# Kernel optimization log

Hardware: AMD Instinct MI355X
Metric: run time of the kernel (lower is better)

Reference implementation:

```python
import jax, jax.numpy as jnp
import numpy as np

N, E, NG, H, BD, L, B = 4000, 50000, 12, 128, 128, 2, 100

def _gelu(x):
    return jax.nn.gelu(x, approximate=False)

def forward(pos, vel, charges, grid0, rand_SO3, batch, edge_index,
            W_basis1, b_basis1, W_basis2, b_basis2,
            W_fbasis1, b_fbasis1, W_fbasis2, b_fbasis2,
            W_embed, W_conv, W_fiber, b_conv, ln_gamma, ln_beta,
            W_ff1, b_ff1, W_ff2, b_ff2, W_ro1, b_ro1, W_ro2, b_ro2):
    n_nodes = pos.shape[0]
    n_graphs = rand_SO3.shape[0]
    n = grid0.shape[0]
    src, dst = edge_index[0], edge_index[1]
    # per-graph randomly rotated S2 grid
    grid_graph = jnp.einsum('bij,nj->bni', rand_SO3, grid0)    # [B,n,3]
    grid_node = grid_graph[batch]                               # [N,n,3]
    grid_edge = grid_node[src]                                  # [E,n,3]
    # R3S2 Euclidean invariants (separable): parallel + perpendicular parts of rel_pos wrt each grid orientation
    rel = pos[src] - pos[dst]                                   # [E,3]
    inv1 = jnp.einsum('ed,end->en', rel, grid_edge)[..., None]  # [E,n,1]
    inv2 = jnp.linalg.norm(rel[:, None, :] - inv1 * grid_edge, axis=-1, keepdims=True)
    cp = (charges[src] * charges[dst])[:, None, :]              # [E,1,1]
    ei = jnp.concatenate([inv1, inv2, jnp.broadcast_to(cp, inv1.shape)], -1)  # [E,n,3]
    # PolynomialFeatures(degree=2): [x, flatten(x outer x)] -> 3+9=12
    ei_poly = jnp.concatenate([ei, (ei[..., :, None] * ei[..., None, :]).reshape(ei.shape[:-1] + (9,))], -1)
    basis = _gelu(_gelu(ei_poly @ W_basis1 + b_basis1) @ W_basis2 + b_basis2)  # [E,n,BD]
    # fiber invariants: pairwise grid dot products (rotation cancels) -> [n,n,1]; poly deg 2 -> [n,n,2]
    fi = jnp.sum(grid0[:, None, :] * grid0[None, :, :], -1, keepdims=True)
    fi_poly = jnp.concatenate([fi, fi * fi], -1)
    fiber_basis = _gelu(_gelu(fi_poly @ W_fbasis1 + b_fbasis1) @ W_fbasis2 + b_fbasis2)  # [n,n,BD]
    # node features projected to sphere
    ones = jnp.ones((n_nodes, 1), pos.dtype)
    cnt = jax.ops.segment_sum(ones, batch, num_segments=n_graphs)
    mean_pos = jax.ops.segment_sum(pos, batch, num_segments=n_graphs) / jnp.maximum(cnt, 1.0)
    rel_pos = pos - mean_pos[batch]
    v_sph = jnp.einsum('nd,nkd->nk', vel, grid_node)[..., None]
    p_sph = jnp.einsum('nd,nkd->nk', rel_pos, grid_node)[..., None]
    c_sph = jnp.broadcast_to(charges[:, None, :], (n_nodes, n, 1))
    vn = jnp.linalg.norm(vel, axis=-1, keepdims=True)
    vn_sph = jnp.broadcast_to(vn[:, None, :], (n_nodes, n, 1))
    x = jnp.concatenate([v_sph, p_sph, c_sph, vn_sph], -1) @ W_embed  # [N,n,H]
    # SeparableBundleConvNext stack
    for l in range(W_conv.shape[0]):
        kern = basis @ W_conv[l]                                       # [E,n,H]
        x1 = jax.ops.segment_sum(x[src] * kern, dst, num_segments=n_nodes)  # depthwise spatial conv + scatter-add
        fk = fiber_basis @ W_fiber[l]                                  # [n,n,H]
        x2 = jnp.einsum('boc,poc->bpc', x1, fk) / n + b_conv[l]        # depthwise fiber conv
        mu = jnp.mean(x2, -1, keepdims=True)
        var = jnp.mean((x2 - mu) ** 2, -1, keepdims=True)
        h = (x2 - mu) / jnp.sqrt(var + 1e-5) * ln_gamma[l] + ln_beta[l]
        h = _gelu(h @ W_ff1[l] + b_ff1[l]) @ W_ff2[l] + b_ff2[l]
        x = x + h
    y = _gelu(x @ W_ro1 + b_ro1) @ W_ro2 + b_ro2                       # [N,n,1]
    return jnp.mean(grid_node * y, axis=-2)                            # sphere2vec -> [N,3]

def setup_inputs():
    key = jax.random.key(0)
    ks = jax.random.split(key, 24)
    f = jnp.float32
    # deterministic uniform-ish S2 grid (fibonacci sphere)
    i = np.arange(NG) + 0.5
    phi = np.arccos(1.0 - 2.0 * i / NG)
    th = np.pi * (1.0 + 5.0 ** 0.5) * i
    grid0 = jnp.asarray(np.stack([np.sin(phi) * np.cos(th), np.sin(phi) * np.sin(th), np.cos(phi)], -1), f)
    # random SO(3) per graph via unit quaternions
    q = jax.random.normal(ks[0], (B, 4), f)
    q = q / jnp.linalg.norm(q, axis=-1, keepdims=True)
    w, xq, yq, zq = q[:, 0], q[:, 1], q[:, 2], q[:, 3]
    R = jnp.stack([
        jnp.stack([1 - 2 * (yq ** 2 + zq ** 2), 2 * (xq * yq - zq * w), 2 * (xq * zq + yq * w)], -1),
        jnp.stack([2 * (xq * yq + zq * w), 1 - 2 * (xq ** 2 + zq ** 2), 2 * (yq * zq - xq * w)], -1),
        jnp.stack([2 * (xq * zq - yq * w), 2 * (yq * zq + xq * w), 1 - 2 * (xq ** 2 + yq ** 2)], -1)], -2)
    s = 0.05
    return dict(
        pos=jax.random.normal(ks[1], (N, 3), f),
        vel=jax.random.normal(ks[2], (N, 3), f),
        charges=jax.random.normal(ks[3], (N, 1), f),
        batch=jnp.sort(jax.random.randint(ks[4], (N,), 0, B)),
        edge_index=jax.random.randint(ks[5], (2, E), 0, N),
        grid0=grid0, rand_SO3=R,
        W_basis1=jax.random.normal(ks[6], (12, H), f) * s, b_basis1=jnp.zeros((H,), f),
        W_basis2=jax.random.normal(ks[7], (H, BD), f) * s, b_basis2=jnp.zeros((BD,), f),
        W_fbasis1=jax.random.normal(ks[8], (2, H), f) * s, b_fbasis1=jnp.zeros((H,), f),
        W_fbasis2=jax.random.normal(ks[9], (H, BD), f) * s, b_fbasis2=jnp.zeros((BD,), f),
        W_embed=jax.random.normal(ks[10], (4, H), f) * s,
        W_conv=jax.random.normal(ks[11], (L, BD, H), f) * s,
        W_fiber=jax.random.normal(ks[12], (L, BD, H), f) * s,
        b_conv=jnp.zeros((L, H), f),
        ln_gamma=jnp.ones((L, H), f), ln_beta=jnp.zeros((L, H), f),
        W_ff1=jax.random.normal(ks[13], (L, H, 4 * H), f) * s, b_ff1=jnp.zeros((L, 4 * H), f),
        W_ff2=jax.random.normal(ks[14], (L, 4 * H, H), f) * s, b_ff2=jnp.zeros((L, H), f),
        W_ro1=jax.random.normal(ks[15], (H, H), f) * s, b_ro1=jnp.zeros((H,), f),
        W_ro2=jax.random.normal(ks[16], (H, 1), f) * s, b_ro2=jnp.zeros((1,), f),
    )

def reference(pos, vel, charges, batch, edge_index, grid0, rand_SO3,
              W_basis1, b_basis1, W_basis2, b_basis2,
              W_fbasis1, b_fbasis1, W_fbasis2, b_fbasis2,
              W_embed, W_conv, W_fiber, b_conv, ln_gamma, ln_beta,
              W_ff1, b_ff1, W_ff2, b_ff2, W_ro1, b_ro1, W_ro2, b_ro2):
    return forward(pos, vel, charges, grid0, rand_SO3, batch, edge_index,
                   W_basis1, b_basis1, W_basis2, b_basis2,
                   W_fbasis1, b_fbasis1, W_fbasis2, b_fbasis2,
                   W_embed, W_conv, W_fiber, b_conv, ln_gamma, ln_beta,
                   W_ff1, b_ff1, W_ff2, b_ff2, W_ro1, b_ro1, W_ro2, b_ro2)
```

## Files before the change

### kernel.cpp

```cpp
#include <hip/hip_runtime.h>

typedef unsigned short u16;
typedef short s16x8 __attribute__((ext_vector_type(8)));
typedef float f32x4 __attribute__((ext_vector_type(4)));

constexpr int NNODES = 4000;
constexpr int NEDGES = 50000;
constexpr int NGRID  = 12;
constexpr int HD     = 128;
constexpr int H4     = 512;
constexpr int NLAY   = 2;

constexpr size_t OFF_GN   = 0;
constexpr size_t OFF_PS   = 144000;
constexpr size_t OFF_CNT  = 144304;
constexpr size_t OFF_FK   = 144512;
constexpr size_t OFF_X    = 181376;
constexpr size_t OFF_X1   = 6325376;
constexpr size_t OFF_WB   = 12469376;
constexpr size_t OFF_ROWP = 12625024;
constexpr size_t OFF_DEG  = 12629032;
constexpr size_t OFF_CUR  = 12633032;
constexpr size_t OFF_ESRT = 12637032;
constexpr size_t OFF_EIPB = 12687032;
constexpr size_t OFF_W1T  = 17487416;
constexpr size_t OFF_SRCS = 17489464;
constexpr size_t OFF_END_SLOW = 17539464;
constexpr size_t OFF_BAS  = 17539464;
constexpr size_t KERN_F   = 38400000;
constexpr size_t OFF_END_FAST  = OFF_BAS + KERN_F;
constexpr size_t OFF_END_DUAL  = OFF_BAS + 2*KERN_F;

constexpr size_t WB_W2T = 0;
constexpr size_t WB_WCT = 16384;
constexpr size_t WB_F1T = 49152;
constexpr size_t WB_F2T = 180224;

__device__ __forceinline__ u16 f2bf(float f){
  union { float f; unsigned int i; } v; v.f = f;
  unsigned int x = v.i;
  x += 0x7fffu + ((x >> 16) & 1u);
  return (u16)(x >> 16);
}
__device__ __forceinline__ float bf2f(u16 u){
  union { unsigned int i; float f; } v; v.i = ((unsigned int)u) << 16; return v.f;
}
__device__ __forceinline__ float gelu_f(float x){
  float z = fabsf(x) * 0.70710678118654752f;
  float t = 1.0f / (1.0f + 0.3275911f * z);
  float p = t*(0.254829592f + t*(-0.284496736f + t*(1.421413741f + t*(-1.453152027f + t*1.061405429f))));
  float erfc_z = p * __expf(-z*z);
  float phi = (x >= 0.0f) ? (1.0f - 0.5f*erfc_z) : (0.5f*erfc_z);
  return x * phi;
}
__device__ __forceinline__ float waveReduceSum(float v){
  #pragma unroll
  for(int off = 32; off > 0; off >>= 1) v += __shfl_xor(v, off, 64);
  return v;
}
__device__ __forceinline__ f32x4 mfma16(s16x8 a, s16x8 b, f32x4 c){
  return __builtin_amdgcn_mfma_f32_16x16x32_bf16(a, b, c, 0, 0, 0);
}

__global__ void k_stats(const float* __restrict__ pos, const int* __restrict__ batch,
                        float* __restrict__ possum, float* __restrict__ pcnt){
  int n = blockIdx.x * 256 + threadIdx.x;
  if(n >= NNODES) return;
  int b = batch[n];
  atomicAdd(&possum[b*3+0], pos[n*3+0]);
  atomicAdd(&possum[b*3+1], pos[n*3+1]);
  atomicAdd(&possum[b*3+2], pos[n*3+2]);
  atomicAdd(&pcnt[b], 1.0f);
}

__global__ void k_gridnode(const float* __restrict__ g0, const float* __restrict__ R,
                           const int* __restrict__ batch, float* __restrict__ grid_node){
  int idx = blockIdx.x * 256 + threadIdx.x;
  if(idx >= NNODES*NGRID) return;
  int n = idx / NGRID, k = idx % NGRID;
  int b = batch[n];
  float g[3];
  #pragma unroll
  for(int j=0;j<3;j++) g[j] = g0[k*3+j];
  #pragma unroll
  for(int i=0;i<3;i++){
    float s = 0.f;
    #pragma unroll
    for(int j=0;j<3;j++) s += R[b*9+i*3+j] * g[j];
    grid_node[idx*3+i] = s;
  }
}

__global__ __launch_bounds__(128) void k_embed(
    const float* __restrict__ pos, const float* __restrict__ vel, const float* __restrict__ charges,
    const int* __restrict__ batch, const float* __restrict__ possum, const float* __restrict__ pcnt,
    const float* __restrict__ grid_node, const float* __restrict__ W_embed, float* __restrict__ x)
{
  int n = blockIdx.x; int t = threadIdx.x;
  __shared__ float feats[NGRID][4];
  __shared__ float sgn[NGRID][3];
  if(t < 36) sgn[t/3][t%3] = grid_node[n*36 + t];
  __syncthreads();
  if(t < NGRID){
    int b = batch[n];
    float inv = 1.0f / fmaxf(pcnt[b], 1.0f);
    float v0=vel[n*3], v1=vel[n*3+1], v2=vel[n*3+2];
    float p0=pos[n*3]   - possum[b*3]*inv;
    float p1=pos[n*3+1] - possum[b*3+1]*inv;
    float p2=pos[n*3+2] - possum[b*3+2]*inv;
    float g0=sgn[t][0], g1=sgn[t][1], g2=sgn[t][2];
    feats[t][0] = v0*g0 + v1*g1 + v2*g2;
    feats[t][1] = p0*g0 + p1*g1 + p2*g2;
    feats[t][2] = charges[n];
    feats[t][3] = sqrtf(v0*v0 + v1*v1 + v2*v2);
  }
  __syncthreads();
  float w0=W_embed[0*HD+t], w1=W_embed[1*HD+t];
  float w2=W_embed[2*HD+t], w3=W_embed[3*HD+t];
  #pragma unroll
  for(int k=0;k<NGRID;k++)
    x[(n*NGRID+k)*HD + t] = feats[k][0]*w0 + feats[k][1]*w1 + feats[k][2]*w2 + feats[k][3]*w3;
}

__global__ __launch_bounds__(128) void k_fiber(
    const float* __restrict__ g0, const float* __restrict__ Wf1, const float* __restrict__ bfb1,
    const float* __restrict__ Wf2, const float* __restrict__ bfb2, const float* __restrict__ W_fiber,
    float* __restrict__ fk)
{
  int po = blockIdx.x; int p = po / NGRID, o = po % NGRID; int c = threadIdx.x;
  __shared__ float st[HD];
  __shared__ float sfb[HD];
  float fi = 0.f;
  #pragma unroll
  for(int j=0;j<3;j++) fi += g0[p*3+j] * g0[o*3+j];
  float f2 = fi*fi;
  st[c] = gelu_f(fi*Wf1[c] + f2*Wf1[HD+c] + bfb1[c]);
  __syncthreads();
  float a = bfb2[c];
  for(int j=0;j<HD;j++) a += st[j] * Wf2[j*HD+c];
  sfb[c] = gelu_f(a);
  __syncthreads();
  for(int l=0;l<NLAY;l++){
    float s = 0.f;
    for(int j=0;j<HD;j++) s += sfb[j] * W_fiber[l*HD*HD + j*HD + c];
    fk[(l*144 + po)*HD + c] = s;
  }
}

__global__ void k_prep(const float* __restrict__ W_b2, const float* __restrict__ W_b1,
                       const float* __restrict__ W_conv, const float* __restrict__ W_ff1,
                       const float* __restrict__ W_ff2,
                       u16* __restrict__ W2T, u16* __restrict__ W1T, u16* __restrict__ WCT,
                       u16* __restrict__ F1T, u16* __restrict__ F2T){
  int idx = blockIdx.x * 256 + threadIdx.x;
  if(idx < 16384){
    int r = idx >> 7, c = idx & 127;
    W2T[c*128 + r] = f2bf(W_b2[idx]);
    return;
  }
  idx -= 16384;
  if(idx < 4096){
    int c = idx >> 5, f = idx & 31;
    W1T[idx] = (f < 12) ? f2bf(W_b1[f*HD + c]) : (u16)0;
    return;
  }
  idx -= 4096;
  if(idx < 32768){
    int l = idx >> 14, j = idx & 16383;
    int r = j >> 7, c = j & 127;
    WCT[l*16384 + c*128 + r] = f2bf(W_conv[l*16384 + j]);
    return;
  }
  idx -= 32768;
  if(idx < 131072){
    int l = idx >> 16, j = idx & 65535;
    int r = j / 512, c = j % 512;
    F1T[l*65536 + c*128 + r] = f2bf(W_ff1[l*65536 + j]);
    return;
  }
  idx -= 131072;
  if(idx < 131072){
    int l = idx >> 16, j = idx & 65535;
    int r = j / 128, c = j % 128;
    F2T[l*65536 + c*512 + r] = f2bf(W_ff2[l*65536 + j]);
  }
}

__global__ void k_prepro(const float* __restrict__ W_ro1, u16* __restrict__ RO1T){
  int idx = blockIdx.x * 256 + threadIdx.x;
  if(idx >= 16384) return;
  int r = idx >> 7, c = idx & 127;
  RO1T[c*128 + r] = f2bf(W_ro1[idx]);
}

__global__ void k_deg(const int* __restrict__ eidx, int* __restrict__ deg){
  int e = blockIdx.x * 256 + threadIdx.x;
  if(e >= NEDGES) return;
  atomicAdd(&deg[eidx[NEDGES + e]], 1);
}

__global__ __launch_bounds__(256) void k_scan(const int* __restrict__ deg, int* __restrict__ rowptr){
  int t = threadIdx.x;
  __shared__ int part[256];
  int base = t * 16;
  int lp[16]; int s = 0;
  #pragma unroll
  for(int i=0;i<16;i++){
    int idx = base + i;
    int v = (idx < NNODES) ? deg[idx] : 0;
    lp[i] = s; s += v;
  }
  part[t] = s;
  __syncthreads();
  for(int off=1; off<256; off<<=1){
    int v2 = (t >= off) ? part[t-off] : 0;
    __syncthreads();
    part[t] += v2;
    __syncthreads();
  }
  int excl = part[t] - s;
  #pragma unroll
  for(int i=0;i<16;i++){
    int idx = base + i;
    if(idx < NNODES) rowptr[idx] = excl + lp[i];
  }
  if(t == 255) rowptr[NNODES] = part[255];
}

__global__ void k_bucket(const int* __restrict__ eidx, const int* __restrict__ rowptr,
                         int* __restrict__ cur, int* __restrict__ esorted, int* __restrict__ srcs){
  int e = blockIdx.x * 256 + threadIdx.x;
  if(e >= NEDGES) return;
  int d = eidx[NEDGES + e];
  int p = atomicAdd(&cur[d], 1);
  int slot = rowptr[d] + p;
  esorted[slot] = e;
  srcs[slot] = eidx[e];
}

__global__ void k_einv(const int* __restrict__ esorted, const int* __restrict__ eidx,
                       const float* __restrict__ pos, const float* __restrict__ charges,
                       const float* __restrict__ grid_node, u16* __restrict__ eipb){
  int row = blockIdx.x * 256 + threadIdx.x;
  if(row >= NEDGES*NGRID) return;
  int p = row / NGRID, kg = row - p*NGRID;
  int e = esorted[p];
  int sr = eidx[e], ds = eidx[NEDGES + e];
  float r0 = pos[sr*3]   - pos[ds*3];
  float r1 = pos[sr*3+1] - pos[ds*3+1];
  float r2 = pos[sr*3+2] - pos[ds*3+2];
  float cp = charges[sr] * charges[ds];
  float g0 = grid_node[sr*36 + kg*3];
  float g1 = grid_node[sr*36 + kg*3 + 1];
  float g2 = grid_node[sr*36 + kg*3 + 2];
  float inv1 = r0*g0 + r1*g1 + r2*g2;
  float d0 = r0 - inv1*g0, d1 = r1 - inv1*g1, d2 = r2 - inv1*g2;
  float inv2 = sqrtf(d0*d0 + d1*d1 + d2*d2);
  float ei[3] = {inv1, inv2, cp};
  s16x8 lo, hi;
  #pragma unroll
  for(int i=0;i<3;i++) lo[i] = (short)f2bf(ei[i]);
  lo[3] = (short)f2bf(ei[0]*ei[0]);
  lo[4] = (short)f2bf(ei[0]*ei[1]);
  lo[5] = (short)f2bf(ei[0]*ei[2]);
  lo[6] = (short)f2bf(ei[1]*ei[0]);
  lo[7] = (short)f2bf(ei[1]*ei[1]);
  hi[0] = (short)f2bf(ei[1]*ei[2]);
  hi[1] = (short)f2bf(ei[2]*ei[0]);
  hi[2] = (short)f2bf(ei[2]*ei[1]);
  hi[3] = (short)f2bf(ei[2]*ei[2]);
  hi[4] = 0; hi[5] = 0; hi[6] = 0; hi[7] = 0;
  *(s16x8*)&eipb[(size_t)row*16]     = lo;
  *(s16x8*)&eipb[(size_t)row*16 + 8] = hi;
}

constexpr int T1S = 136;

__global__ __launch_bounds__(256) void k_kern(
    const u16* __restrict__ eipb, const u16* __restrict__ W1T,
    const float* __restrict__ b1, const float* __restrict__ b2,
    const u16* __restrict__ W2T, const u16* __restrict__ WCT,
    u16* __restrict__ kern, int nl, size_t kstride)
{
  int t = threadIdx.x;
  int lane = t & 63, w = t >> 6, quad = lane >> 4, l16 = lane & 15;
  size_t R0 = (size_t)blockIdx.x * 64;
  __shared__ __align__(16) u16 s_buf[64*T1S];

  float b1v[2], b2v[2];
  #pragma unroll
  for(int nt=0;nt<2;nt++){
    b1v[nt] = b1[(2*w+nt)*16 + l16];
    b2v[nt] = b2[(2*w+nt)*16 + l16];
  }
  const s16x8 zvec = {0,0,0,0,0,0,0,0};

  {
    f32x4 a1[4][2];
    #pragma unroll
    for(int mt=0;mt<4;mt++)
      #pragma unroll
      for(int nt=0;nt<2;nt++) a1[mt][nt] = (f32x4){0.f,0.f,0.f,0.f};
    s16x8 Af[4];
    #pragma unroll
    for(int mt=0;mt<4;mt++){
      s16x8 v = *(const s16x8*)&eipb[(R0 + mt*16 + l16)*16 + (quad&1)*8];
      if(quad >= 2) v = zvec;
      Af[mt] = v;
    }
    #pragma unroll
    for(int nt=0;nt<2;nt++){
      s16x8 Bf = *(const s16x8*)&W1T[((2*w+nt)*16 + l16)*32 + quad*8];
      #pragma unroll
      for(int mt=0;mt<4;mt++) a1[mt][nt] = mfma16(Af[mt], Bf, a1[mt][nt]);
    }
    #pragma unroll
    for(int mt=0;mt<4;mt++)
      #pragma unroll
      for(int nt=0;nt<2;nt++)
        #pragma unroll
        for(int i=0;i<4;i++)
          s_buf[(mt*16 + quad*4 + i)*T1S + (2*w+nt)*16 + l16] = f2bf(gelu_f(a1[mt][nt][i] + b1v[nt]));
  }
  __syncthreads();
  f32x4 a2[4][2];
  #pragma unroll
  for(int mt=0;mt<4;mt++)
    #pragma unroll
    for(int nt=0;nt<2;nt++) a2[mt][nt] = (f32x4){0.f,0.f,0.f,0.f};
  #pragma unroll
  for(int ks=0; ks<4; ks++){
    s16x8 Af[4];
    #pragma unroll
    for(int mt=0;mt<4;mt++)
      Af[mt] = *(const s16x8*)&s_buf[(mt*16 + l16)*T1S + ks*32 + quad*8];
    #pragma unroll
    for(int nt=0;nt<2;nt++){
      s16x8 Bf = *(const s16x8*)&W2T[((2*w+nt)*16 + l16)*HD + ks*32 + quad*8];
      #pragma unroll
      for(int mt=0;mt<4;mt++) a2[mt][nt] = mfma16(Af[mt], Bf, a2[mt][nt]);
    }
  }
  __syncthreads();
  #pragma unroll
  for(int mt=0;mt<4;mt++)
    #pragma unroll
    for(int nt=0;nt<2;nt++)
      #pragma unroll
      for(int i=0;i<4;i++)
        s_buf[(mt*16 + quad*4 + i)*T1S + (2*w+nt)*16 + l16] = f2bf(gelu_f(a2[mt][nt][i] + b2v[nt]));
  __syncthreads();
  for(int l=0; l<nl; l++){
    f32x4 a3[4][2];
    #pragma unroll
    for(int mt=0;mt<4;mt++)
      #pragma unroll
      for(int nt=0;nt<2;nt++) a3[mt][nt] = (f32x4){0.f,0.f,0.f,0.f};
    #pragma unroll
    for(int ks=0; ks<4; ks++){
      s16x8 Af[4];
      #pragma unroll
      for(int mt=0;mt<4;mt++)
        Af[mt] = *(const s16x8*)&s_buf[(mt*16 + l16)*T1S + ks*32 + quad*8];
      #pragma unroll
      for(int nt=0;nt<2;nt++){
        s16x8 Bf = *(const s16x8*)&WCT[l*16384 + ((2*w+nt)*16 + l16)*HD + ks*32 + quad*8];
        #pragma unroll
        for(int mt=0;mt<4;mt++) a3[mt][nt] = mfma16(Af[mt], Bf, a3[mt][nt]);
      }
    }
    #pragma unroll
    for(int mt=0;mt<4;mt++)
      #pragma unroll
      for(int nt=0;nt<2;nt++)
        #pragma unroll
        for(int i=0;i<4;i++)
          kern[l*kstride + (R0 + mt*16 + quad*4 + i)*HD + (2*w+nt)*16 + l16] = f2bf(a3[mt][nt][i]);
  }
}

__global__ __launch_bounds__(256) void k_gather(
    const u16* __restrict__ kern, const float* __restrict__ x,
    const int* __restrict__ rowptr, const int* __restrict__ srcs,
    const float* __restrict__ fkl, const float* __restrict__ bconv,
    const float* __restrict__ gamma, const float* __restrict__ beta,
    u16* __restrict__ hout)
{
  int n = blockIdx.x, t = threadIdx.x;
  int c = t & 127, half = t >> 7;
  int w = t >> 6, lane = t & 63;
  __shared__ float raw[NGRID*HD];
  __shared__ float red[4][6], red2[4][6];
  int base = rowptr[n];
  int d = rowptr[n+1] - base;
  float acc[6] = {0.f,0.f,0.f,0.f,0.f,0.f};
  int srcn = (d > 0) ? srcs[base] : 0;
  for(int e=0; e<d; e++){
    int nsrc = (e+1 < d) ? srcs[base+e+1] : 0;
    const u16*   kp = &kern[((size_t)(base+e)*NGRID + half*6)*HD + c];
    const float* xp = &x[((size_t)srcn*NGRID + half*6)*HD + c];
    #pragma unroll
    for(int kk=0;kk<6;kk++)
      acc[kk] += bf2f(kp[kk*HD]) * xp[kk*HD];
    srcn = nsrc;
  }
  #pragma unroll
  for(int kk=0;kk<6;kk++)
    raw[(half*6+kk)*HD + c] = acc[kk];
  __syncthreads();
  float bc = bconv[c];
  float v[6];
  #pragma unroll
  for(int kk=0;kk<6;kk++){
    int p = half*6 + kk;
    float a = 0.f;
    #pragma unroll
    for(int o=0;o<NGRID;o++)
      a += raw[o*HD + c] * fkl[(p*NGRID+o)*HD + c];
    v[kk] = a * (1.0f/12.0f) + bc;
  }
  #pragma unroll
  for(int kk=0;kk<6;kk++){
    float s = waveReduceSum(v[kk]);
    if(lane == 0) red[w][kk] = s;
  }
  __syncthreads();
  float dd[6];
  #pragma unroll
  for(int kk=0;kk<6;kk++){
    float mu = (red[half*2][kk] + red[half*2+1][kk]) * (1.0f/128.0f);
    dd[kk] = v[kk] - mu;
    float s2 = waveReduceSum(dd[kk]*dd[kk]);
    if(lane == 0) red2[w][kk] = s2;
  }
  __syncthreads();
  float ga = gamma[c], be = beta[c];
  #pragma unroll
  for(int kk=0;kk<6;kk++){
    float var = (red2[half*2][kk] + red2[half*2+1][kk]) * (1.0f/128.0f);
    float inv = 1.0f / sqrtf(var + 1e-5f);
    hout[((size_t)n*NGRID + half*6 + kk)*HD + c] = f2bf(dd[kk] * inv * ga + be);
  }
}

__global__ __launch_bounds__(256) void k_ff1(
    const u16* __restrict__ F1T, const float* __restrict__ bf1,
    const u16* __restrict__ hin, u16* __restrict__ h4)
{
  int t = threadIdx.x;
  size_t r0 = (size_t)blockIdx.x * 32;
  int lane = t & 63, w = t >> 6, quad = lane >> 4, l16 = lane & 15;
  __shared__ __align__(16) u16 sxh[32*T1S];
  for(int i=t; i<32*HD/8; i+=256){
    int r = (i*8) >> 7, cc = (i*8) & 127;
    *(s16x8*)&sxh[r*T1S + cc] = *(const s16x8*)&hin[r0*HD + (size_t)i*8];
  }
  __syncthreads();
  f32x4 acc[2][8];
  #pragma unroll
  for(int mt=0;mt<2;mt++)
    #pragma unroll
    for(int j=0;j<8;j++) acc[mt][j] = (f32x4){0.f,0.f,0.f,0.f};
  #pragma unroll
  for(int ks=0; ks<4; ks++){
    s16x8 Af0 = *(const s16x8*)&sxh[l16*T1S + ks*32 + quad*8];
    s16x8 Af1 = *(const s16x8*)&sxh[(16 + l16)*T1S + ks*32 + quad*8];
    #pragma unroll
    for(int j=0;j<8;j++){
      int nt = w*8 + j;
      s16x8 Bf = *(const s16x8*)&F1T[((size_t)(nt*16 + l16))*HD + ks*32 + quad*8];
      acc[0][j] = mfma16(Af0, Bf, acc[0][j]);
      acc[1][j] = mfma16(Af1, Bf, acc[1][j]);
    }
  }
  #pragma unroll
  for(int j=0;j<8;j++){
    int col = (w*8+j)*16 + l16;
    float bv = bf1[col];
    #pragma unroll
    for(int mt=0;mt<2;mt++)
      #pragma unroll
      for(int i=0;i<4;i++){
        int row = mt*16 + quad*4 + i;
        h4[(r0 + row)*H4 + col] = f2bf(gelu_f(acc[mt][j][i] + bv));
      }
  }
}

__global__ __launch_bounds__(256) void k_ff2(
    const u16* __restrict__ F2T, const float* __restrict__ bf2,
    const u16* __restrict__ h4, float* __restrict__ x)
{
  int t = threadIdx.x;
  size_t r0 = (size_t)blockIdx.x * 32;
  int lane = t & 63, w = t >> 6, quad = lane >> 4, l16 = lane & 15;
  f32x4 acc[2][2];
  #pragma unroll
  for(int mt=0;mt<2;mt++)
    #pragma unroll
    for(int j=0;j<2;j++) acc[mt][j] = (f32x4){0.f,0.f,0.f,0.f};
  for(int ks=0; ks<16; ks++){
    s16x8 Af0 = *(const s16x8*)&h4[(r0 + l16)*H4 + ks*32 + quad*8];
    s16x8 Af1 = *(const s16x8*)&h4[(r0 + 16 + l16)*H4 + ks*32 + quad*8];
    #pragma unroll
    for(int j=0;j<2;j++){
      int nt = w*2 + j;
      s16x8 Bf = *(const s16x8*)&F2T[((size_t)(nt*16 + l16))*H4 + ks*32 + quad*8];
      acc[0][j] = mfma16(Af0, Bf, acc[0][j]);
      acc[1][j] = mfma16(Af1, Bf, acc[1][j]);
    }
  }
  #pragma unroll
  for(int j=0;j<2;j++){
    int col = (w*2+j)*16 + l16;
    float bv = bf2[col];
    #pragma unroll
    for(int mt=0;mt<2;mt++)
      #pragma unroll
      for(int i=0;i<4;i++){
        size_t row = r0 + mt*16 + quad*4 + i;
        x[row*HD + col] += acc[mt][j][i] + bv;
      }
  }
}

__global__ __launch_bounds__(256) void k_conv_slow(
    const u16* __restrict__ eipb, const u16* __restrict__ W1T,
    const float* __restrict__ b1, const float* __restrict__ b2,
    const u16* __restrict__ W2T, const u16* __restrict__ WCT,
    const float* __restrict__ x,
    const int* __restrict__ rowptr, const int* __restrict__ srcs,
    float* __restrict__ x1o)
{
  int n = blockIdx.x; int t = threadIdx.x;
  int lane = t & 63, w = t >> 6, quad = lane >> 4, l16 = lane & 15;

  __shared__ __align__(16) u16 s_t1h[48*T1S];
  __shared__ __align__(16) u16 s_bas[48*T1S];
  __shared__ __align__(16) float accLDS[NGRID*HD];

  int base = rowptr[n];
  int d = rowptr[n+1] - base;

  float b1v[2], b2v[2];
  #pragma unroll
  for(int nt=0;nt<2;nt++){
    b1v[nt] = b1[(2*w+nt)*16 + l16];
    b2v[nt] = b2[(2*w+nt)*16 + l16];
  }

  for(int i=t; i<NGRID*HD; i+=256) accLDS[i] = 0.f;
  __syncthreads();

  f32x4 accv[3][2];
  #pragma unroll
  for(int mt=0;mt<3;mt++)
    #pragma unroll
    for(int nt=0;nt<2;nt++) accv[mt][nt] = (f32x4){0.f,0.f,0.f,0.f};

  const s16x8 zvec = {0,0,0,0,0,0,0,0};

  for(int ch=0; ch<d; ch+=4){
    size_t rowb = (size_t)(base + ch) * NGRID;
    s16x8 Af1[3];
    #pragma unroll
    for(int mt=0;mt<3;mt++){
      s16x8 v = *(const s16x8*)&eipb[(rowb + mt*16 + l16)*16 + (quad&1)*8];
      if(quad >= 2) v = zvec;
      Af1[mt] = v;
    }
    float xv[3][4][2];
    #pragma unroll
    for(int mt=0;mt<3;mt++)
      #pragma unroll
      for(int i=0;i<4;i++){
        int row = mt*16 + quad*4 + i;
        int e = row / 12;
        int k = row - e*12;
        int ei2 = base + ch + e;
        int srcn = srcs[min(ei2, NEDGES-1)];
        float m = (ch + e < d) ? 1.0f : 0.0f;
        const float* xp = &x[((size_t)srcn*NGRID + k)*HD + l16];
        #pragma unroll
        for(int nt=0;nt<2;nt++)
          xv[mt][i][nt] = xp[(2*w+nt)*16] * m;
      }
    {
      f32x4 a1[3][2];
      #pragma unroll
      for(int mt=0;mt<3;mt++)
        #pragma unroll
        for(int nt=0;nt<2;nt++) a1[mt][nt] = (f32x4){0.f,0.f,0.f,0.f};
      #pragma unroll
      for(int nt=0;nt<2;nt++){
        s16x8 Bf = *(const s16x8*)&W1T[((2*w+nt)*16 + l16)*32 + quad*8];
        #pragma unroll
        for(int mt=0;mt<3;mt++) a1[mt][nt] = mfma16(Af1[mt], Bf, a1[mt][nt]);
      }
      #pragma unroll
      for(int mt=0;mt<3;mt++)
        #pragma unroll
        for(int nt=0;nt<2;nt++)
          #pragma unroll
          for(int i=0;i<4;i++)
            s_t1h[(mt*16 + quad*4 + i)*T1S + (2*w+nt)*16 + l16] = f2bf(gelu_f(a1[mt][nt][i] + b1v[nt]));
    }
    __syncthreads();
    {
      f32x4 a2[3][2];
      #pragma unroll
      for(int mt=0;mt<3;mt++)
        #pragma unroll
        for(int nt=0;nt<2;nt++) a2[mt][nt] = (f32x4){0.f,0.f,0.f,0.f};
      #pragma unroll
      for(int ks=0; ks<4; ks++){
        s16x8 Af[3];
        #pragma unroll
        for(int mt=0;mt<3;mt++)
          Af[mt] = *(const s16x8*)&s_t1h[(mt*16 + l16)*T1S + ks*32 + quad*8];
        #pragma unroll
        for(int nt=0;nt<2;nt++){
          s16x8 Bf = *(const s16x8*)&W2T[((2*w+nt)*16 + l16)*HD + ks*32 + quad*8];
          #pragma unroll
          for(int mt=0;mt<3;mt++) a2[mt][nt] = mfma16(Af[mt], Bf, a2[mt][nt]);
        }
      }
      #pragma unroll
      for(int mt=0;mt<3;mt++)
        #pragma unroll
        for(int nt=0;nt<2;nt++)
          #pragma unroll
          for(int i=0;i<4;i++)
            s_bas[(mt*16 + quad*4 + i)*T1S + (2*w+nt)*16 + l16] = f2bf(gelu_f(a2[mt][nt][i] + b2v[nt]));
    }
    __syncthreads();
    {
      f32x4 a3[3][2];
      #pragma unroll
      for(int mt=0;mt<3;mt++)
        #pragma unroll
        for(int nt=0;nt<2;nt++) a3[mt][nt] = (f32x4){0.f,0.f,0.f,0.f};
      #pragma unroll
      for(int ks=0; ks<4; ks++){
        s16x8 Af[3];
        #pragma unroll
        for(int mt=0;mt<3;mt++)
          Af[mt] = *(const s16x8*)&s_bas[(mt*16 + l16)*T1S + ks*32 + quad*8];
        #pragma unroll
        for(int nt=0;nt<2;nt++){
          s16x8 Bf = *(const s16x8*)&WCT[((2*w+nt)*16 + l16)*HD + ks*32 + quad*8];
          #pragma unroll
          for(int mt=0;mt<3;mt++) a3[mt][nt] = mfma16(Af[mt], Bf, a3[mt][nt]);
        }
      }
      #pragma unroll
      for(int mt=0;mt<3;mt++)
        #pragma unroll
        for(int nt=0;nt<2;nt++)
          #pragma unroll
          for(int i=0;i<4;i++)
            accv[mt][nt][i] += a3[mt][nt][i] * xv[mt][i][nt];
    }
  }
  __syncthreads();
  #pragma unroll
  for(int mt=0;mt<3;mt++)
    #pragma unroll
    for(int nt=0;nt<2;nt++)
      #pragma unroll
      for(int i=0;i<4;i++){
        int row = mt*16 + quad*4 + i;
        int k = row % 12;
        atomicAdd(&accLDS[k*HD + (2*w+nt)*16 + l16], accv[mt][nt][i]);
      }
  __syncthreads();
  for(int i=t; i<NGRID*HD; i+=256)
    x1o[(size_t)n*NGRID*HD + i] = accLDS[i];
}

constexpr int STS = 520;
__global__ __launch_bounds__(256) void k_ffln(
    const u16* __restrict__ F1T, const float* __restrict__ bf1,
    const u16* __restrict__ F2T, const float* __restrict__ bf2,
    const float* __restrict__ x1raw,
    const float* __restrict__ fkl, const float* __restrict__ bconv,
    const float* __restrict__ gamma, const float* __restrict__ beta,
    float* __restrict__ x)
{
  int n = blockIdx.x; int t = threadIdx.x;
  int lane = t & 63, w = t >> 6, quad = lane >> 4, l16 = lane & 15;
  __shared__ __align__(16) float raw[NGRID*HD];
  __shared__ __align__(16) u16 sxh[16*T1S];
  __shared__ __align__(16) u16 st[16*STS];

  for(int i=t; i<NGRID*HD; i+=256) raw[i] = x1raw[(size_t)n*NGRID*HD + i];
  for(int i=t; i<4*T1S; i+=256) sxh[12*T1S + i] = 0;
  __syncthreads();

  {
    int c0 = lane, c1 = lane + 64;
    float bc0 = bconv[c0], bc1 = bconv[c1];
    float ga0 = gamma[c0], ga1 = gamma[c1];
    float be0 = beta[c0],  be1 = beta[c1];
    #pragma unroll
    for(int pp=0; pp<3; pp++){
      int p = w + pp*4;
      float a0 = 0.f, a1 = 0.f;
      #pragma unroll
      for(int o=0;o<NGRID;o++){
        a0 += raw[o*HD + c0] * fkl[(p*NGRID+o)*HD + c0];
        a1 += raw[o*HD + c1] * fkl[(p*NGRID+o)*HD + c1];
      }
      float v0 = a0 * (1.0f/12.0f) + bc0;
      float v1 = a1 * (1.0f/12.0f) + bc1;
      float mu = waveReduceSum(v0 + v1) * (1.0f/128.0f);
      float d0 = v0 - mu, d1 = v1 - mu;
      float var = waveReduceSum(d0*d0 + d1*d1) * (1.0f/128.0f);
      float inv = 1.0f / sqrtf(var + 1e-5f);
      sxh[p*T1S + c0] = f2bf(d0 * inv * ga0 + be0);
      sxh[p*T1S + c1] = f2bf(d1 * inv * ga1 + be1);
    }
  }
  __syncthreads();
  {
    f32x4 acc1[8];
    #pragma unroll
    for(int j=0;j<8;j++) acc1[j] = (f32x4){0.f,0.f,0.f,0.f};
    #pragma unroll
    for(int ks=0; ks<4; ks++){
      s16x8 Af = *(const s16x8*)&sxh[l16*T1S + ks*32 + quad*8];
      #pragma unroll
      for(int j=0;j<8;j++){
        int nt = w*8 + j;
        s16x8 Bf = *(const s16x8*)&F1T[((size_t)(nt*16 + l16))*HD + ks*32 + quad*8];
        acc1[j] = mfma16(Af, Bf, acc1[j]);
      }
    }
    #pragma unroll
    for(int j=0;j<8;j++){
      int col = (w*8+j)*16 + l16;
      float bv = bf1[col];
      #pragma unroll
      for(int i=0;i<4;i++){
        int row = quad*4 + i;
        st[row*STS + col] = f2bf(gelu_f(acc1[j][i] + bv));
      }
    }
  }
  __syncthreads();
  {
    f32x4 acc2[2];
    #pragma unroll
    for(int j=0;j<2;j++) acc2[j] = (f32x4){0.f,0.f,0.f,0.f};
    for(int ks=0; ks<16; ks++){
      s16x8 Af = *(const s16x8*)&st[l16*STS + ks*32 + quad*8];
      #pragma unroll
      for(int j=0;j<2;j++){
        int nt = w*2 + j;
        s16x8 Bf = *(const s16x8*)&F2T[((size_t)(nt*16 + l16))*H4 + ks*32 + quad*8];
        acc2[j] = mfma16(Af, Bf, acc2[j]);
      }
    }
    #pragma unroll
    for(int j=0;j<2;j++){
      int col = (w*2+j)*16 + l16;
      float bv = bf2[col];
      #pragma unroll
      for(int i=0;i<4;i++){
        int row = quad*4 + i;
        if(row < NGRID){
          size_t idx = ((size_t)n*NGRID + row)*HD + col;
          x[idx] += acc2[j][i] + bv;
        }
      }
    }
  }
}

__global__ __launch_bounds__(256) void k_readout(
    const float* __restrict__ x, const float* __restrict__ grid_node,
    const u16* __restrict__ RO1T, const float* __restrict__ br1,
    const float* __restrict__ Wr2, const float* __restrict__ br2,
    float* __restrict__ out)
{
  int t = threadIdx.x;
  int n0 = blockIdx.x * 2;
  int lane = t & 63, w = t >> 6, quad = lane >> 4, l16 = lane & 15;
  __shared__ __align__(16) u16 sxh[32*T1S];
  __shared__ float sy[32];
  if(t < 32) sy[t] = 0.f;
  for(int i=t; i<2*NGRID*HD; i+=256){
    int nd = i / (NGRID*HD), rem = i - nd*NGRID*HD;
    int r = rem >> 7, c = rem & 127;
    sxh[(nd*16 + r)*T1S + c] = f2bf(x[(size_t)n0*NGRID*HD + i]);
  }
  for(int i=t; i<4*T1S; i+=256){ sxh[12*T1S + i] = 0; sxh[28*T1S + i] = 0; }
  __syncthreads();
  f32x4 acc[2][2];
  #pragma unroll
  for(int mt=0;mt<2;mt++)
    #pragma unroll
    for(int j=0;j<2;j++) acc[mt][j] = (f32x4){0.f,0.f,0.f,0.f};
  #pragma unroll
  for(int ks=0; ks<4; ks++){
    s16x8 Af0 = *(const s16x8*)&sxh[l16*T1S + ks*32 + quad*8];
    s16x8 Af1 = *(const s16x8*)&sxh[(16 + l16)*T1S + ks*32 + quad*8];
    #pragma unroll
    for(int j=0;j<2;j++){
      int nt = w*2 + j;
      s16x8 Bf = *(const s16x8*)&RO1T[((size_t)(nt*16 + l16))*HD + ks*32 + quad*8];
      acc[0][j] = mfma16(Af0, Bf, acc[0][j]);
      acc[1][j] = mfma16(Af1, Bf, acc[1][j]);
    }
  }
  #pragma unroll
  for(int j=0;j<2;j++){
    int col = (w*2+j)*16 + l16;
    float bv = br1[col];
    float w2v = Wr2[col];
    #pragma unroll
    for(int mt=0;mt<2;mt++)
      #pragma unroll
      for(int i=0;i<4;i++){
        int row = quad*4 + i;
        if(row < NGRID)
          atomicAdd(&sy[mt*16 + row], gelu_f(acc[mt][j][i] + bv) * w2v);
      }
  }
  __syncthreads();
  if(t < 6){
    int nd = t / 3, d = t - nd*3;
    float b2v = br2[0];
    float s = 0.f;
    #pragma unroll
    for(int k=0;k<NGRID;k++)
      s += grid_node[((size_t)(n0+nd)*NGRID + k)*3 + d] * (sy[nd*16 + k] + b2v);
    out[(n0+nd)*3 + d] = s * (1.0f/12.0f);
  }
}

extern "C" void kernel_launch(void* const* d_in, const int* in_sizes, int n_in,
                              void* d_out, int out_size, void* d_ws, size_t ws_size,
                              hipStream_t stream)
{
  const float* pos      = (const float*)d_in[0];
  const float* vel      = (const float*)d_in[1];
  const float* charges  = (const float*)d_in[2];
  const int*   batch    = (const int*)d_in[3];
  const int*   eidx     = (const int*)d_in[4];
  const float* grid0    = (const float*)d_in[5];
  const float* R        = (const float*)d_in[6];
  const float* W_b1     = (const float*)d_in[7];
  const float* b_b1     = (const float*)d_in[8];
  const float* W_b2     = (const float*)d_in[9];
  const float* b_b2     = (const float*)d_in[10];
  const float* W_fb1    = (const float*)d_in[11];
  const float* b_fb1    = (const float*)d_in[12];
  const float* W_fb2    = (const float*)d_in[13];
  const float* b_fb2    = (const float*)d_in[14];
  const float* W_embed  = (const float*)d_in[15];
  const float* W_conv   = (const float*)d_in[16];
  const float* W_fiber  = (const float*)d_in[17];
  const float* b_conv   = (const float*)d_in[18];
  const float* ln_g     = (const float*)d_in[19];
  const float* ln_b     = (const float*)d_in[20];
  const float* W_ff1    = (const float*)d_in[21];
  const float* b_ff1    = (const float*)d_in[22];
  const float* W_ff2    = (const float*)d_in[23];
  const float* b_ff2    = (const float*)d_in[24];
  const float* W_ro1    = (const float*)d_in[25];
  const float* b_ro1    = (const float*)d_in[26];
  const float* W_ro2    = (const float*)d_in[27];
  const float* b_ro2    = (const float*)d_in[28];

  float* ws        = (float*)d_ws;
  float* grid_node = ws + OFF_GN;
  float* possum    = ws + OFF_PS;
  float* pcnt      = ws + OFF_CNT;
  float* fk        = ws + OFF_FK;
  float* x         = ws + OFF_X;
  float* x1        = ws + OFF_X1;
  u16*   WB        = (u16*)(ws + OFF_WB);
  u16*   W2T       = WB + WB_W2T;
  u16*   WCT       = WB + WB_WCT;
  u16*   F1T       = WB + WB_F1T;
  u16*   F2T       = WB + WB_F2T;
  int*   rowptr    = (int*)(ws + OFF_ROWP);
  int*   deg       = (int*)(ws + OFF_DEG);
  int*   cur       = (int*)(ws + OFF_CUR);
  int*   esorted   = (int*)(ws + OFF_ESRT);
  u16*   eipb      = (u16*)(ws + OFF_EIPB);
  u16*   W1T       = (u16*)(ws + OFF_W1T);
  int*   srcs      = (int*)(ws + OFF_SRCS);
  u16*   kern1     = (u16*)(ws + OFF_BAS);
  u16*   RO1T      = (u16*)(ws + OFF_ESRT);
  u16*   hbuf      = (u16*)x1;
  const size_t KSTR = (size_t)600000 * HD;

  const bool fast = (ws_size >= OFF_END_FAST * sizeof(float));
  const bool dual = (ws_size >= OFF_END_DUAL * sizeof(float));

  hipMemsetAsync(possum, 0, 512*sizeof(float), stream);
  hipMemsetAsync(deg, 0, NNODES*sizeof(int), stream);
  hipMemsetAsync(cur, 0, NNODES*sizeof(int), stream);
  hipMemsetAsync(eipb + (size_t)NEDGES*NGRID*16, 0, 48*16*sizeof(u16), stream);

  k_stats<<<(NNODES+255)/256, 256, 0, stream>>>(pos, batch, possum, pcnt);
  k_gridnode<<<(NNODES*NGRID+255)/256, 256, 0, stream>>>(grid0, R, batch, grid_node);
  k_embed<<<NNODES, 128, 0, stream>>>(pos, vel, charges, batch, possum, pcnt, grid_node, W_embed, x);
  k_fiber<<<144, 128, 0, stream>>>(grid0, W_fb1, b_fb1, W_fb2, b_fb2, W_fiber, fk);

  k_prep<<<(315392+255)/256, 256, 0, stream>>>(W_b2, W_b1, W_conv, W_ff1, W_ff2,
                                               W2T, W1T, WCT, F1T, F2T);

  k_deg<<<(NEDGES+255)/256, 256, 0, stream>>>(eidx, deg);
  k_scan<<<1, 256, 0, stream>>>(deg, rowptr);
  k_bucket<<<(NEDGES+255)/256, 256, 0, stream>>>(eidx, rowptr, cur, esorted, srcs);

  k_einv<<<(NEDGES*NGRID+255)/256, 256, 0, stream>>>(esorted, eidx, pos, charges, grid_node, eipb);
  k_prepro<<<64, 256, 0, stream>>>(W_ro1, RO1T);

  if(fast){
    if(dual)
      k_kern<<<9375, 256, 0, stream>>>(eipb, W1T, b_b1, b_b2, W2T, WCT, kern1, 2, KSTR);
    for(int l=0; l<NLAY; l++){
      if(!dual)
        k_kern<<<9375, 256, 0, stream>>>(eipb, W1T, b_b1, b_b2, W2T, WCT + (size_t)l*16384,
                                         kern1, 1, 0);
      const u16* kl = dual ? (kern1 + (size_t)l*KSTR) : kern1;
      u16* h4 = dual ? (kern1 + (size_t)l*KSTR) : kern1;
      k_gather<<<NNODES, 256, 0, stream>>>(kl, x, rowptr, srcs,
          fk + (size_t)l*144*HD, b_conv + l*HD, ln_g + l*HD, ln_b + l*HD, hbuf);
      k_ff1<<<NNODES*NGRID/32, 256, 0, stream>>>(F1T + (size_t)l*65536, b_ff1 + l*H4, hbuf, h4);
      k_ff2<<<NNODES*NGRID/32, 256, 0, stream>>>(F2T + (size_t)l*65536, b_ff2 + l*HD, h4, x);
    }
  } else {
    for(int l=0; l<NLAY; l++){
      k_conv_slow<<<NNODES, 256, 0, stream>>>(eipb, W1T, b_b1, b_b2, W2T, WCT + (size_t)l*16384,
          x, rowptr, srcs, x1);
      k_ffln<<<NNODES, 256, 0, stream>>>(F1T + (size_t)l*65536, b_ff1 + l*H4,
          F2T + (size_t)l*65536, b_ff2 + l*HD, x1,
          fk + (size_t)l*144*HD, b_conv + l*HD, ln_g + l*HD, ln_b + l*HD, x);
    }
  }

  k_readout<<<NNODES/2, 256, 0, stream>>>(x, grid_node, RO1T, b_ro1, W_ro2, b_ro2, (float*)d_out);
}
```

Baseline: 820.5 us.

## Fuse small setup kernels, merge dual-layer conv MFMA loop, use erff GELU

Folds the node-stats and degree-count kernels into one launch, and moves grid-node rotation into the weight prep kernel, cutting launch count. The two deg and cur memsets are merged into one, which relies on the two arrays being adjacent in the workspace. In the basis kernel the two conv-layer projections now share each A-fragment load and run in one interleaved MFMA loop, at the cost of twice as many accumulator registers. GELU switches from the polynomial erfc approximation to the library erff, which may cost more instructions per call.

```diff
diff --git a/kernel.cpp b/kernel.cpp
--- a/kernel.cpp
+++ b/kernel.cpp
@@ -46,12 +46,7 @@
   union { unsigned int i; float f; } v; v.i = ((unsigned int)u) << 16; return v.f;
 }
 __device__ __forceinline__ float gelu_f(float x){
-  float z = fabsf(x) * 0.70710678118654752f;
-  float t = 1.0f / (1.0f + 0.3275911f * z);
-  float p = t*(0.254829592f + t*(-0.284496736f + t*(1.421413741f + t*(-1.453152027f + t*1.061405429f))));
-  float erfc_z = p * __expf(-z*z);
-  float phi = (x >= 0.0f) ? (1.0f - 0.5f*erfc_z) : (0.5f*erfc_z);
-  return x * phi;
+  return 0.5f * x * (1.0f + erff(x * 0.70710678118654752f));
 }
 __device__ __forceinline__ float waveReduceSum(float v){
   #pragma unroll
@@ -62,33 +57,20 @@
   return __builtin_amdgcn_mfma_f32_16x16x32_bf16(a, b, c, 0, 0, 0);
 }
 
-__global__ void k_stats(const float* __restrict__ pos, const int* __restrict__ batch,
-                        float* __restrict__ possum, float* __restrict__ pcnt){
-  int n = blockIdx.x * 256 + threadIdx.x;
-  if(n >= NNODES) return;
-  int b = batch[n];
-  atomicAdd(&possum[b*3+0], pos[n*3+0]);
-  atomicAdd(&possum[b*3+1], pos[n*3+1]);
-  atomicAdd(&possum[b*3+2], pos[n*3+2]);
-  atomicAdd(&pcnt[b], 1.0f);
-}
-
-__global__ void k_gridnode(const float* __restrict__ g0, const float* __restrict__ R,
-                           const int* __restrict__ batch, float* __restrict__ grid_node){
-  int idx = blockIdx.x * 256 + threadIdx.x;
-  if(idx >= NNODES*NGRID) return;
-  int n = idx / NGRID, k = idx % NGRID;
-  int b = batch[n];
-  float g[3];
-  #pragma unroll
-  for(int j=0;j<3;j++) g[j] = g0[k*3+j];
-  #pragma unroll
-  for(int i=0;i<3;i++){
-    float s = 0.f;
-    #pragma unroll
-    for(int j=0;j<3;j++) s += R[b*9+i*3+j] * g[j];
-    grid_node[idx*3+i] = s;
-  }
+__global__ void k_statdeg(const float* __restrict__ pos, const int* __restrict__ batch,
+                          const int* __restrict__ eidx,
+                          float* __restrict__ possum, float* __restrict__ pcnt,
+                          int* __restrict__ deg){
+  int i = blockIdx.x * 256 + threadIdx.x;
+  if(i < NNODES){
+    int b = batch[i];
+    atomicAdd(&possum[b*3+0], pos[i*3+0]);
+    atomicAdd(&possum[b*3+1], pos[i*3+1]);
+    atomicAdd(&possum[b*3+2], pos[i*3+2]);
+    atomicAdd(&pcnt[b], 1.0f);
+  }
+  int e = i - NNODES;
+  if(e >= 0 && e < NEDGES) atomicAdd(&deg[eidx[NEDGES + e]], 1);
 }
 
 __global__ __launch_bounds__(128) void k_embed(
@@ -147,12 +129,30 @@
   }
 }
 
-__global__ void k_prep(const float* __restrict__ W_b2, const float* __restrict__ W_b1,
+__global__ void k_prep(const float* __restrict__ g0, const float* __restrict__ R,
+                       const int* __restrict__ batch, float* __restrict__ grid_node,
+                       const float* __restrict__ W_b2, const float* __restrict__ W_b1,
                        const float* __restrict__ W_conv, const float* __restrict__ W_ff1,
                        const float* __restrict__ W_ff2,
                        u16* __restrict__ W2T, u16* __restrict__ W1T, u16* __restrict__ WCT,
                        u16* __restrict__ F1T, u16* __restrict__ F2T){
   int idx = blockIdx.x * 256 + threadIdx.x;
+  if(idx < NNODES*NGRID){
+    int n = idx / NGRID, k = idx % NGRID;
+    int b = batch[n];
+    float g[3];
+    #pragma unroll
+    for(int j=0;j<3;j++) g[j] = g0[k*3+j];
+    #pragma unroll
+    for(int i=0;i<3;i++){
+      float s = 0.f;
+      #pragma unroll
+      for(int j=0;j<3;j++) s += R[b*9+i*3+j] * g[j];
+      grid_node[idx*3+i] = s;
+    }
+    return;
+  }
+  idx -= NNODES*NGRID;
   if(idx < 16384){
     int r = idx >> 7, c = idx & 127;
     W2T[c*128 + r] = f2bf(W_b2[idx]);
@@ -185,18 +185,13 @@
     F2T[l*65536 + c*512 + r] = f2bf(W_ff2[l*65536 + j]);
   }
 }
+constexpr int PREP_N = NNODES*NGRID + 16384 + 4096 + 32768 + 131072 + 131072;
 
 __global__ void k_prepro(const float* __restrict__ W_ro1, u16* __restrict__ RO1T){
   int idx = blockIdx.x * 256 + threadIdx.x;
   if(idx >= 16384) return;
   int r = idx >> 7, c = idx & 127;
   RO1T[c*128 + r] = f2bf(W_ro1[idx]);
-}
-
-__global__ void k_deg(const int* __restrict__ eidx, int* __restrict__ deg){
-  int e = blockIdx.x * 256 + threadIdx.x;
-  if(e >= NEDGES) return;
-  atomicAdd(&deg[eidx[NEDGES + e]], 1);
 }
 
 __global__ __launch_bounds__(256) void k_scan(const int* __restrict__ deg, int* __restrict__ rowptr){
@@ -350,12 +345,14 @@
       for(int i=0;i<4;i++)
         s_buf[(mt*16 + quad*4 + i)*T1S + (2*w+nt)*16 + l16] = f2bf(gelu_f(a2[mt][nt][i] + b2v[nt]));
   __syncthreads();
-  for(int l=0; l<nl; l++){
-    f32x4 a3[4][2];
+  if(nl == 2){
+    f32x4 a3[4][2][2];
     #pragma unroll
     for(int mt=0;mt<4;mt++)
       #pragma unroll
-      for(int nt=0;nt<2;nt++) a3[mt][nt] = (f32x4){0.f,0.f,0.f,0.f};
+      for(int nt=0;nt<2;nt++)
+        #pragma unroll
+        for(int l=0;l<2;l++) a3[mt][nt][l] = (f32x4){0.f,0.f,0.f,0.f};
     #pragma unroll
     for(int ks=0; ks<4; ks++){
       s16x8 Af[4];
@@ -364,7 +361,39 @@
         Af[mt] = *(const s16x8*)&s_buf[(mt*16 + l16)*T1S + ks*32 + quad*8];
       #pragma unroll
       for(int nt=0;nt<2;nt++){
-        s16x8 Bf = *(const s16x8*)&WCT[l*16384 + ((2*w+nt)*16 + l16)*HD + ks*32 + quad*8];
+        s16x8 Bf0 = *(const s16x8*)&WCT[((2*w+nt)*16 + l16)*HD + ks*32 + quad*8];
+        s16x8 Bf1 = *(const s16x8*)&WCT[16384 + ((2*w+nt)*16 + l16)*HD + ks*32 + quad*8];
+        #pragma unroll
+        for(int mt=0;mt<4;mt++){
+          a3[mt][nt][0] = mfma16(Af[mt], Bf0, a3[mt][nt][0]);
+          a3[mt][nt][1] = mfma16(Af[mt], Bf1, a3[mt][nt][1]);
+        }
+      }
+    }
+    #pragma unroll
+    for(int l=0;l<2;l++)
+      #pragma unroll
+      for(int mt=0;mt<4;mt++)
+        #pragma unroll
+        for(int nt=0;nt<2;nt++)
+          #pragma unroll
+          for(int i=0;i<4;i++)
+            kern[l*kstride + (R0 + mt*16 + quad*4 + i)*HD + (2*w+nt)*16 + l16] = f2bf(a3[mt][nt][l][i]);
+  } else {
+    f32x4 a3[4][2];
+    #pragma unroll
+    for(int mt=0;mt<4;mt++)
+      #pragma unroll
+      for(int nt=0;nt<2;nt++) a3[mt][nt] = (f32x4){0.f,0.f,0.f,0.f};
+    #pragma unroll
+    for(int ks=0; ks<4; ks++){
+      s16x8 Af[4];
+      #pragma unroll
+      for(int mt=0;mt<4;mt++)
+        Af[mt] = *(const s16x8*)&s_buf[(mt*16 + l16)*T1S + ks*32 + quad*8];
+      #pragma unroll
+      for(int nt=0;nt<2;nt++){
+        s16x8 Bf = *(const s16x8*)&WCT[((2*w+nt)*16 + l16)*HD + ks*32 + quad*8];
         #pragma unroll
         for(int mt=0;mt<4;mt++) a3[mt][nt] = mfma16(Af[mt], Bf, a3[mt][nt]);
       }
@@ -375,7 +404,7 @@
       for(int nt=0;nt<2;nt++)
         #pragma unroll
         for(int i=0;i<4;i++)
-          kern[l*kstride + (R0 + mt*16 + quad*4 + i)*HD + (2*w+nt)*16 + l16] = f2bf(a3[mt][nt][i]);
+          kern[(R0 + mt*16 + quad*4 + i)*HD + (2*w+nt)*16 + l16] = f2bf(a3[mt][nt][i]);
   }
 }
 
@@ -901,19 +930,16 @@
   const bool dual = (ws_size >= OFF_END_DUAL * sizeof(float));
 
   hipMemsetAsync(possum, 0, 512*sizeof(float), stream);
-  hipMemsetAsync(deg, 0, NNODES*sizeof(int), stream);
-  hipMemsetAsync(cur, 0, NNODES*sizeof(int), stream);
+  hipMemsetAsync(deg, 0, 2*NNODES*sizeof(int), stream);
   hipMemsetAsync(eipb + (size_t)NEDGES*NGRID*16, 0, 48*16*sizeof(u16), stream);
 
-  k_stats<<<(NNODES+255)/256, 256, 0, stream>>>(pos, batch, possum, pcnt);
-  k_gridnode<<<(NNODES*NGRID+255)/256, 256, 0, stream>>>(grid0, R, batch, grid_node);
+  k_statdeg<<<(NNODES+NEDGES+255)/256, 256, 0, stream>>>(pos, batch, eidx, possum, pcnt, deg);
+  k_prep<<<(PREP_N+255)/256, 256, 0, stream>>>(grid0, R, batch, grid_node,
+                                               W_b2, W_b1, W_conv, W_ff1, W_ff2,
+                                               W2T, W1T, WCT, F1T, F2T);
   k_embed<<<NNODES, 128, 0, stream>>>(pos, vel, charges, batch, possum, pcnt, grid_node, W_embed, x);
   k_fiber<<<144, 128, 0, stream>>>(grid0, W_fb1, b_fb1, W_fb2, b_fb2, W_fiber, fk);
 
-  k_prep<<<(315392+255)/256, 256, 0, stream>>>(W_b2, W_b1, W_conv, W_ff1, W_ff2,
-                                               W2T, W1T, WCT, F1T, F2T);
-
-  k_deg<<<(NEDGES+255)/256, 256, 0, stream>>>(eidx, deg);
   k_scan<<<1, 256, 0, stream>>>(deg, rowptr);
   k_bucket<<<(NEDGES+255)/256, 256, 0, stream>>>(eidx, rowptr, cur, esorted, srcs);
 
```

New measurement: 910.6 us. 11.0% more time.
